# Kernel optimization log

Hardware: AMD Instinct MI355X
Metric: run time of the kernel (lower is better)

The kernel has to match this reference:

```python
import jax, jax.numpy as jnp
import numpy as np

INPUT, HIDDEN, LINEAR, BATCH, SEQ = 300, 1024, 1024, 256, 128
EPS = 1e-5

def setup_inputs() -> dict:
    key = jax.random.key(0)
    ks = jax.random.split(key, 12)
    s_ih = 1.0 / np.sqrt(HIDDEN)
    inp = {
        "x": jax.random.normal(ks[0], (SEQ, BATCH, INPUT), dtype=jnp.float32),
        "W_ih": jax.random.uniform(ks[1], (4 * HIDDEN, INPUT), jnp.float32, -s_ih, s_ih),
        "W_hh": jax.random.uniform(ks[2], (4 * HIDDEN, HIDDEN), jnp.float32, -s_ih, s_ih),
        "b_ih": jax.random.uniform(ks[3], (4 * HIDDEN,), jnp.float32, -s_ih, s_ih),
        "b_hh": jax.random.uniform(ks[4], (4 * HIDDEN,), jnp.float32, -s_ih, s_ih),
        "W1": jax.random.uniform(ks[5], (LINEAR, HIDDEN), jnp.float32, -s_ih, s_ih),
        "b1": jax.random.uniform(ks[6], (LINEAR,), jnp.float32, -s_ih, s_ih),
        "gamma": jnp.ones((LINEAR,), jnp.float32),
        "beta": jnp.zeros((LINEAR,), jnp.float32),
        "W2": jax.random.uniform(ks[7], (1, LINEAR), jnp.float32, -1.0 / np.sqrt(LINEAR), 1.0 / np.sqrt(LINEAR)),
        "b2": jax.random.uniform(ks[8], (1,), jnp.float32, -1.0 / np.sqrt(LINEAR), 1.0 / np.sqrt(LINEAR)),
    }
    return inp

def reference(x, W_ih, W_hh, b_ih, b_hh, W1, b1, gamma, beta, W2, b2):
    # Stepwise LSTMCell loop (dropout path; training=False -> dropout is identity)
    B, H = x.shape[1], W_hh.shape[1]
    bias = b_ih + b_hh  # [4H]

    def step(carry, xt):
        h, c = carry
        gates = xt @ W_ih.T + h @ W_hh.T + bias  # [B, 4H]
        i, f, g, o = jnp.split(gates, 4, axis=-1)
        c = jax.nn.sigmoid(f) * c + jax.nn.sigmoid(i) * jnp.tanh(g)
        h = jax.nn.sigmoid(o) * jnp.tanh(c)
        return (h, c), None

    h0 = jnp.zeros((B, H), x.dtype)
    (h, _), _ = jax.lax.scan(step, (h0, h0), x)

    # head: linear -> BatchNorm1d (train-mode batch stats) -> relu -> linear
    z = h @ W1.T + b1  # [B, LINEAR]
    mean = jnp.mean(z, axis=0)
    var = jnp.var(z, axis=0)  # biased, matching torch BN training path
    z = (z - mean) * jax.lax.rsqrt(var + EPS) * gamma + beta
    z = jax.nn.relu(z)
    out = z @ W2.T + b2  # [B, 1]
    out = 3.0 * jax.nn.sigmoid(out)
    return out.squeeze(-1)  # [B]
```

## Files before the change

kernel.cpp:

```cpp
#include <hip/hip_runtime.h>
#include <math.h>

#define SEQ 128
#define BATCH 256
#define INPUT 300
#define HIDDEN 1024
#define NG 4096
#define KH 1024
#define KXP 320
#define KT 1344
#define NKT64 21
#define HT64 16
#define NKTH 32
#define LINEARN 1024
#define AROW 72
#define TILE_SH (64 * AROW)
#define BUF_SH (3 * TILE_SH)

typedef __attribute__((ext_vector_type(8))) short short8;
typedef __attribute__((ext_vector_type(4))) float floatx4;

__device__ __forceinline__ float sigf(float x)     { return 1.f / (1.f + __expf(-x)); }
__device__ __forceinline__ float tanhfast(float x) { return 2.f / (1.f + __expf(-2.f * x)) - 1.f; }

__device__ __forceinline__ unsigned short bf16_rne(float f) {
  unsigned u = __float_as_uint(f);
  u += 0x7FFFu + ((u >> 16) & 1u);
  return (unsigned short)(u >> 16);
}
__device__ __forceinline__ float bf16f(unsigned short s) {
  return __uint_as_float(((unsigned)s) << 16);
}

__device__ __forceinline__ void mfma3(floatx4& acc, short8 ah, short8 al, short8 bh, short8 bl) {
  acc = __builtin_amdgcn_mfma_f32_16x16x32_bf16(ah, bh, acc, 0, 0, 0);
  acc = __builtin_amdgcn_mfma_f32_16x16x32_bf16(ah, bl, acc, 0, 0, 0);
  acc = __builtin_amdgcn_mfma_f32_16x16x32_bf16(al, bh, acc, 0, 0, 0);
}
__device__ __forceinline__ void mfma2(floatx4& acc, short8 ah, short8 al, short8 bh) {
  acc = __builtin_amdgcn_mfma_f32_16x16x32_bf16(ah, bh, acc, 0, 0, 0);
  acc = __builtin_amdgcn_mfma_f32_16x16x32_bf16(al, bh, acc, 0, 0, 0);
}

__global__ __launch_bounds__(256) void zero_ws(float4* p, int n4) {
  int i = blockIdx.x * 256 + threadIdx.x;
  if (i < n4) p[i] = make_float4(0.f, 0.f, 0.f, 0.f);
}

__global__ __launch_bounds__(256) void pack_w(
    const float* __restrict__ W_ih, const float* __restrict__ W_hh,
    unsigned short* __restrict__ Wph)
{
  int id = blockIdx.x * 256 + threadIdx.x;
  if (id >= NG * KT) return;
  int n = id / KT;
  int k = id - n * KT;
  int j = n >> 2, g = n & 3;
  int srow = g * HIDDEN + j;
  float w = 0.f;
  if (k < KH) w = W_hh[(size_t)srow * HIDDEN + k];
  else if (k - KH < INPUT) w = W_ih[(size_t)srow * INPUT + (k - KH)];
  Wph[id] = bf16_rne(w);
}

__global__ __launch_bounds__(256) void pack_bias(
    const float* __restrict__ b_ih, const float* __restrict__ b_hh,
    float* __restrict__ biasp)
{
  int n = blockIdx.x * 256 + threadIdx.x;
  if (n >= NG) return;
  int j = n >> 2, g = n & 3;
  int s = g * HIDDEN + j;
  biasp[n] = b_ih[s] + b_hh[s];
}

__global__ __launch_bounds__(256) void pack_x(
    const float* __restrict__ x, unsigned short* __restrict__ xph,
    unsigned short* __restrict__ xpl)
{
  int id = blockIdx.x * 256 + threadIdx.x;
  if (id >= SEQ * BATCH * KXP) return;
  int row = id / KXP;
  int k = id - row * KXP;
  float v = (k < INPUT) ? x[(size_t)row * INPUT + k] : 0.f;
  unsigned short hi = bf16_rne(v);
  xph[id] = hi;
  xpl[id] = bf16_rne(v - bf16f(hi));
}

__global__ __launch_bounds__(256) void pack_w1(
    const float* __restrict__ W1, unsigned short* __restrict__ W1ph,
    unsigned short* __restrict__ W1pl)
{
  int id = blockIdx.x * 256 + threadIdx.x;
  if (id >= LINEARN * HIDDEN) return;
  float w = W1[id];
  unsigned short hi = bf16_rne(w);
  W1ph[id] = hi;
  W1pl[id] = bf16_rne(w - bf16f(hi));
}

__global__ __launch_bounds__(512) void lstm_step5(
    const unsigned short* __restrict__ xp_hi,
    const unsigned short* __restrict__ xp_lo,
    const unsigned short* __restrict__ h_hi_r,
    const unsigned short* __restrict__ h_lo_r,
    const unsigned short* __restrict__ Wph,
    const float* __restrict__ biasp,
    float* __restrict__ cst,
    unsigned short* __restrict__ h_hi_w,
    unsigned short* __restrict__ h_lo_w)
{
  __shared__ short sb[2 * BUF_SH];
  __shared__ float epi[64 * 65];

  const int t    = threadIdx.x;
  const int lane = t & 63;
  const int wave = t >> 6;
  const int wm   = (wave >> 2) * 32;
  const int wn   = (wave & 3) * 16;
  const int col  = lane & 15;
  const int quad = lane >> 4;
  const int r    = t >> 3;
  const int k8   = (t & 7) * 8;
  const int id     = blockIdx.x;
  const int jtile  = (id & 7) * 8 + ((id >> 3) & 7);
  const int mt_    = id >> 6;
  const int m0   = mt_ * 64;
  const int n0   = jtile * 64;
  const int j0   = jtile * 16;

  const int mloc = t >> 2;
  const int jl4  = (t & 3) * 4;
  float4 cold;
  if (t < 256) cold = *(const float4*)(cst + (size_t)(m0 + mloc) * HIDDEN + (j0 + jl4));

#define LOAD_TILE(kt, AH, AL, BH) do {                                       \
    if ((kt) < HT64) {                                                       \
      const int ka = (kt) * 64 + k8;                                         \
      AH = *(const uint4*)(h_hi_r + (size_t)(m0 + r) * KH + ka);             \
      AL = *(const uint4*)(h_lo_r + (size_t)(m0 + r) * KH + ka);             \
    } else {                                                                 \
      const int kx = ((kt) - HT64) * 64 + k8;                                \
      AH = *(const uint4*)(xp_hi + (size_t)(m0 + r) * KXP + kx);             \
      AL = *(const uint4*)(xp_lo + (size_t)(m0 + r) * KXP + kx);             \
    }                                                                        \
    BH = *(const uint4*)(Wph + (size_t)(n0 + r) * KT + (kt) * 64 + k8);      \
  } while (0)

#define STORE_TILE(base, AH, AL, BH) do {                                    \
    *(uint4*)((base) +               r * AROW + k8) = AH;                    \
    *(uint4*)((base) + TILE_SH     + r * AROW + k8) = AL;                    \
    *(uint4*)((base) + 2 * TILE_SH + r * AROW + k8) = BH;                    \
  } while (0)

  floatx4 acc[2];
  acc[0] = (floatx4){0.f, 0.f, 0.f, 0.f};
  acc[1] = (floatx4){0.f, 0.f, 0.f, 0.f};

  uint4 cAh, cAl, cBh, nAh, nAl, nBh, tAh, tAl, tBh;
  LOAD_TILE(0, tAh, tAl, tBh);
  LOAD_TILE(1, cAh, cAl, cBh);
  STORE_TILE(sb, tAh, tAl, tBh);

  const int arow0 = (wm + col) * AROW + quad * 8;
  const int arow1 = (wm + 16 + col) * AROW + quad * 8;
  const int brow  = (wn + col) * AROW + quad * 8;

  for (int kt = 0; kt < NKT64; ++kt) {
    if (kt + 2 < NKT64) LOAD_TILE(kt + 2, nAh, nAl, nBh);
    __syncthreads();
    const short* bufp = sb + (kt & 1) * BUF_SH;

#pragma unroll
    for (int sub = 0; sub < 2; ++sub) {
      const int so = sub * 32;
      const short8 bh = *(const short8*)(bufp + 2 * TILE_SH + brow + so);
      const short8 a0 = *(const short8*)(bufp + arow0 + so);
      const short8 l0 = *(const short8*)(bufp + TILE_SH + arow0 + so);
      const short8 a1 = *(const short8*)(bufp + arow1 + so);
      const short8 l1 = *(const short8*)(bufp + TILE_SH + arow1 + so);
      mfma2(acc[0], a0, l0, bh);
      mfma2(acc[1], a1, l1, bh);
    }

    if (kt + 1 < NKT64) STORE_TILE(sb + ((kt + 1) & 1) * BUF_SH, cAh, cAl, cBh);
    cAh = nAh; cAl = nAl; cBh = nBh;
  }
#undef LOAD_TILE
#undef STORE_TILE

  const float bb = biasp[n0 + wn + col];
#pragma unroll
  for (int mt = 0; mt < 2; ++mt) {
    const int nl = wn + col;
#pragma unroll
    for (int reg = 0; reg < 4; ++reg) {
      const int ml = wm + mt * 16 + quad * 4 + reg;
      epi[nl * 65 + ml] = acc[mt][reg] + bb;
    }
  }
  __syncthreads();

  if (t < 256) {
    float cn[4], hn[4];
#pragma unroll
    for (int jj = 0; jj < 4; ++jj) {
      const int nl = (jl4 + jj) * 4;
      const float gi = epi[(nl + 0) * 65 + mloc];
      const float gf = epi[(nl + 1) * 65 + mloc];
      const float gg = epi[(nl + 2) * 65 + mloc];
      const float go = epi[(nl + 3) * 65 + mloc];
      const float cc = (jj == 0) ? cold.x : (jj == 1) ? cold.y : (jj == 2) ? cold.z : cold.w;
      const float cnew = sigf(gf) * cc + sigf(gi) * tanhfast(gg);
      cn[jj] = cnew;
      hn[jj] = sigf(go) * tanhfast(cnew);
    }
    *(float4*)(cst + (size_t)(m0 + mloc) * HIDDEN + (j0 + jl4)) =
        make_float4(cn[0], cn[1], cn[2], cn[3]);
    ushort4 uh, ul;
    uh.x = bf16_rne(hn[0]); uh.y = bf16_rne(hn[1]);
    uh.z = bf16_rne(hn[2]); uh.w = bf16_rne(hn[3]);
    ul.x = bf16_rne(hn[0] - bf16f(uh.x));
    ul.y = bf16_rne(hn[1] - bf16f(uh.y));
    ul.z = bf16_rne(hn[2] - bf16f(uh.z));
    ul.w = bf16_rne(hn[3] - bf16f(uh.w));
    *(ushort4*)(h_hi_w + (size_t)(m0 + mloc) * HIDDEN + (j0 + jl4)) = uh;
    *(ushort4*)(h_lo_w + (size_t)(m0 + mloc) * HIDDEN + (j0 + jl4)) = ul;
  }
}

__global__ __launch_bounds__(256) void head_gemm(
    const unsigned short* __restrict__ Ah_,
    const unsigned short* __restrict__ Al_,
    const unsigned short* __restrict__ Bh_,
    const unsigned short* __restrict__ Bl_,
    const float* __restrict__ bias,
    float* __restrict__ C)
{
  __shared__ short sb[2 * 4 * 2560];

  const int t    = threadIdx.x;
  const int lane = t & 63;
  const int wave = t >> 6;
  const int wm   = (wave >> 1) * 32;
  const int wn   = (wave & 1) * 32;
  const int col  = lane & 15;
  const int quad = lane >> 4;
  const int r    = t >> 2;
  const int k8   = (t & 3) * 8;
  const int m0   = blockIdx.y * 64;
  const int n0   = blockIdx.x * 64;

#define LOAD_TILE(kt, AH, AL, BH, BL) do {                                   \
    const int ka = (kt) * 32 + k8;                                           \
    AH = *(const uint4*)(Ah_ + (size_t)(m0 + r) * KH + ka);                  \
    AL = *(const uint4*)(Al_ + (size_t)(m0 + r) * KH + ka);                  \
    BH = *(const uint4*)(Bh_ + (size_t)(n0 + r) * KH + ka);                  \
    BL = *(const uint4*)(Bl_ + (size_t)(n0 + r) * KH + ka);                  \
  } while (0)

#define STORE_TILE(base, AH, AL, BH, BL) do {                                \
    *(uint4*)((base) +        r * 40 + k8) = AH;                             \
    *(uint4*)((base) + 2560 + r * 40 + k8) = AL;                             \
    *(uint4*)((base) + 5120 + r * 40 + k8) = BH;                             \
    *(uint4*)((base) + 7680 + r * 40 + k8) = BL;                             \
  } while (0)

  floatx4 acc[2][2];
#pragma unroll
  for (int i = 0; i < 2; ++i)
#pragma unroll
    for (int jj = 0; jj < 2; ++jj)
      acc[i][jj] = (floatx4){0.f, 0.f, 0.f, 0.f};

  uint4 cAh, cAl, cBh, cBl, nAh, nAl, nBh, nBl, tAh, tAl, tBh, tBl;
  LOAD_TILE(0, tAh, tAl, tBh, tBl);
  LOAD_TILE(1, cAh, cAl, cBh, cBl);
  STORE_TILE(sb, tAh, tAl, tBh, tBl);

  for (int kt = 0; kt < NKTH; ++kt) {
    if (kt + 2 < NKTH) LOAD_TILE(kt + 2, nAh, nAl, nBh, nBl);
    __syncthreads();
    short* bufp = sb + (kt & 1) * 10240;

    short8 ah[2], al[2], bh[2], bl[2];
#pragma unroll
    for (int mt = 0; mt < 2; ++mt) {
      const int row = (wm + mt * 16 + col) * 40 + quad * 8;
      ah[mt] = *(const short8*)(bufp + row);
      al[mt] = *(const short8*)(bufp + 2560 + row);
    }
#pragma unroll
    for (int nt = 0; nt < 2; ++nt) {
      const int row = (wn + nt * 16 + col) * 40 + quad * 8;
      bh[nt] = *(const short8*)(bufp + 5120 + row);
      bl[nt] = *(const short8*)(bufp + 7680 + row);
    }
#pragma unroll
    for (int mt = 0; mt < 2; ++mt)
#pragma unroll
      for (int nt = 0; nt < 2; ++nt)
        mfma3(acc[mt][nt], ah[mt], al[mt], bh[nt], bl[nt]);

    if (kt + 1 < NKTH) STORE_TILE(sb + ((kt + 1) & 1) * 10240, cAh, cAl, cBh, cBl);
    cAh = nAh; cAl = nAl; cBh = nBh; cBl = nBl;
  }
#undef LOAD_TILE
#undef STORE_TILE

#pragma unroll
  for (int mt = 0; mt < 2; ++mt)
#pragma unroll
    for (int nt = 0; nt < 2; ++nt) {
      const int nl = n0 + wn + nt * 16 + col;
      const float bb = bias[nl];
#pragma unroll
      for (int reg = 0; reg < 4; ++reg) {
        const int ml = m0 + wm + mt * 16 + quad * 4 + reg;
        C[(size_t)ml * LINEARN + nl] = acc[mt][nt][reg] + bb;
      }
    }
}

__global__ __launch_bounds__(64) void bn_stats(
    const float* __restrict__ z, float* __restrict__ mean, float* __restrict__ rstd)
{
  const int n = blockIdx.x;
  const int t = threadIdx.x;
  float s = 0.f, s2 = 0.f;
  for (int r = t; r < BATCH; r += 64) {
    const float v = z[(size_t)r * LINEARN + n];
    s += v; s2 += v * v;
  }
#pragma unroll
  for (int off = 32; off > 0; off >>= 1) {
    s  += __shfl_down(s,  off, 64);
    s2 += __shfl_down(s2, off, 64);
  }
  if (t == 0) {
    const float mm = s * (1.f / BATCH);
    mean[n] = mm;
    rstd[n] = rsqrtf(s2 * (1.f / BATCH) - mm * mm + 1e-5f);
  }
}

__global__ __launch_bounds__(256) void head_out(
    const float* __restrict__ z, const float* __restrict__ mean, const float* __restrict__ rstd,
    const float* __restrict__ gamma, const float* __restrict__ beta,
    const float* __restrict__ W2, const float* __restrict__ b2, float* __restrict__ out)
{
  const int b = blockIdx.x;
  const int t = threadIdx.x;
  float acc = 0.f;
  for (int n = t; n < LINEARN; n += 256) {
    float v = (z[(size_t)b * LINEARN + n] - mean[n]) * rstd[n] * gamma[n] + beta[n];
    v = fmaxf(v, 0.f);
    acc += v * W2[n];
  }
#pragma unroll
  for (int off = 32; off > 0; off >>= 1) acc += __shfl_down(acc, off, 64);
  __shared__ float ls[4];
  if ((t & 63) == 0) ls[t >> 6] = acc;
  __syncthreads();
  if (t == 0) {
    const float tot = ls[0] + ls[1] + ls[2] + ls[3] + b2[0];
    out[b] = 3.f / (1.f + __expf(-tot));
  }
}

extern "C" void kernel_launch(void* const* d_in, const int* in_sizes, int n_in,
                              void* d_out, int out_size, void* d_ws, size_t ws_size,
                              hipStream_t stream) {
  const float* x     = (const float*)d_in[0];
  const float* W_ih  = (const float*)d_in[1];
  const float* W_hh  = (const float*)d_in[2];
  const float* b_ih  = (const float*)d_in[3];
  const float* b_hh  = (const float*)d_in[4];
  const float* W1    = (const float*)d_in[5];
  const float* b1    = (const float*)d_in[6];
  const float* gamma = (const float*)d_in[7];
  const float* beta  = (const float*)d_in[8];
  const float* W2    = (const float*)d_in[9];
  const float* b2    = (const float*)d_in[10];
  float* out = (float*)d_out;

  char* w = (char*)d_ws;
  unsigned short* h_hi0 = (unsigned short*)(w + 0);
  unsigned short* h_lo0 = (unsigned short*)(w + 524288);
  float*          cst   = (float*)(w + 1048576);
  unsigned short* h_hi1 = (unsigned short*)(w + 2097152);
  unsigned short* h_lo1 = (unsigned short*)(w + 2621440);
  unsigned short* Wph   = (unsigned short*)(w + 3145728);
  float*          biasp = (float*)(w + 14155776);
  unsigned short* xph   = (unsigned short*)(w + 14172160);
  unsigned short* xpl   = (unsigned short*)(w + 35143680);
  unsigned short* W1ph  = (unsigned short*)(w + 56115200);
  unsigned short* W1pl  = (unsigned short*)(w + 58212352);
  float*          z     = (float*)(w + 60309504);
  float*          mean  = (float*)(w + 61358080);
  float*          rstd  = (float*)(w + 61362176);

  zero_ws<<<512, 256, 0, stream>>>((float4*)w, 131072);
  pack_w<<<(NG * KT + 255) / 256, 256, 0, stream>>>(W_ih, W_hh, Wph);
  pack_bias<<<NG / 256, 256, 0, stream>>>(b_ih, b_hh, biasp);
  pack_x<<<(SEQ * BATCH * KXP + 255) / 256, 256, 0, stream>>>(x, xph, xpl);
  pack_w1<<<(LINEARN * HIDDEN + 255) / 256, 256, 0, stream>>>(W1, W1ph, W1pl);

  for (int t = 0; t < SEQ; ++t) {
    const unsigned short* hr_hi = (t & 1) ? h_hi1 : h_hi0;
    const unsigned short* hr_lo = (t & 1) ? h_lo1 : h_lo0;
    unsigned short* hw_hi = (t & 1) ? h_hi0 : h_hi1;
    unsigned short* hw_lo = (t & 1) ? h_lo0 : h_lo1;
    lstm_step5<<<256, 512, 0, stream>>>(
        xph + (size_t)t * BATCH * KXP, xpl + (size_t)t * BATCH * KXP,
        hr_hi, hr_lo, Wph, biasp, cst, hw_hi, hw_lo);
  }

  head_gemm<<<dim3(LINEARN / 64, BATCH / 64), 256, 0, stream>>>(
      h_hi0, h_lo0, W1ph, W1pl, b1, z);
  bn_stats<<<LINEARN, 64, 0, stream>>>(z, mean, rstd);
  head_out<<<BATCH, 256, 0, stream>>>(z, mean, rstd, gamma, beta, W2, b2, out);
}
```

Before: 1.850 ms.

## Double LSTM step K-tile to 128 and swap wave tiling to share A fragments

The per-step LSTM GEMM now stages 128-wide K tiles instead of 64, halving the number of barrier-synchronised iterations. The padded x width grows from 320 to 384 columns to fit the larger tile, and the workspace offsets are updated to match. Each wave now covers 16 rows by 32 gate columns, so one hi/lo A fragment is reused across two B fragments, cutting LDS reads per MFMA. In exchange, shared memory per block roughly doubles, which may reduce occupancy, and the extra zero padding in K adds some wasted MFMA work.

```diff
diff --git a/kernel.cpp b/kernel.cpp
--- a/kernel.cpp
+++ b/kernel.cpp
@@ -7,13 +7,13 @@
 #define HIDDEN 1024
 #define NG 4096
 #define KH 1024
-#define KXP 320
-#define KT 1344
-#define NKT64 21
-#define HT64 16
+#define KXP 384
+#define KT 1408
+#define NKT128 11
+#define HT128 8
 #define NKTH 32
 #define LINEARN 1024
-#define AROW 72
+#define AROW 136
 #define TILE_SH (64 * AROW)
 #define BUF_SH (3 * TILE_SH)
 
@@ -100,7 +100,7 @@
   W1pl[id] = bf16_rne(w - bf16f(hi));
 }
 
-__global__ __launch_bounds__(512) void lstm_step5(
+__global__ __launch_bounds__(512) void lstm_step6(
     const unsigned short* __restrict__ xp_hi,
     const unsigned short* __restrict__ xp_lo,
     const unsigned short* __restrict__ h_hi_r,
@@ -117,8 +117,8 @@
   const int t    = threadIdx.x;
   const int lane = t & 63;
   const int wave = t >> 6;
-  const int wm   = (wave >> 2) * 32;
-  const int wn   = (wave & 3) * 16;
+  const int wm   = (wave & 3) * 16;
+  const int wn   = (wave >> 2) * 32;
   const int col  = lane & 15;
   const int quad = lane >> 4;
   const int r    = t >> 3;
@@ -135,69 +135,80 @@
   float4 cold;
   if (t < 256) cold = *(const float4*)(cst + (size_t)(m0 + mloc) * HIDDEN + (j0 + jl4));
 
-#define LOAD_TILE(kt, AH, AL, BH) do {                                       \
-    if ((kt) < HT64) {                                                       \
-      const int ka = (kt) * 64 + k8;                                         \
-      AH = *(const uint4*)(h_hi_r + (size_t)(m0 + r) * KH + ka);             \
-      AL = *(const uint4*)(h_lo_r + (size_t)(m0 + r) * KH + ka);             \
+#define LOAD_TILE(kt, AH0, AH1, AL0, AL1, BH0, BH1) do {                     \
+    if ((kt) < HT128) {                                                      \
+      const int ka = (kt) * 128 + k8;                                        \
+      AH0 = *(const uint4*)(h_hi_r + (size_t)(m0 + r) * KH + ka);            \
+      AH1 = *(const uint4*)(h_hi_r + (size_t)(m0 + r) * KH + ka + 64);       \
+      AL0 = *(const uint4*)(h_lo_r + (size_t)(m0 + r) * KH + ka);            \
+      AL1 = *(const uint4*)(h_lo_r + (size_t)(m0 + r) * KH + ka + 64);       \
     } else {                                                                 \
-      const int kx = ((kt) - HT64) * 64 + k8;                                \
-      AH = *(const uint4*)(xp_hi + (size_t)(m0 + r) * KXP + kx);             \
-      AL = *(const uint4*)(xp_lo + (size_t)(m0 + r) * KXP + kx);             \
+      const int kx = ((kt) - HT128) * 128 + k8;                              \
+      AH0 = *(const uint4*)(xp_hi + (size_t)(m0 + r) * KXP + kx);            \
+      AH1 = *(const uint4*)(xp_hi + (size_t)(m0 + r) * KXP + kx + 64);       \
+      AL0 = *(const uint4*)(xp_lo + (size_t)(m0 + r) * KXP + kx);            \
+      AL1 = *(const uint4*)(xp_lo + (size_t)(m0 + r) * KXP + kx + 64);       \
     }                                                                        \
-    BH = *(const uint4*)(Wph + (size_t)(n0 + r) * KT + (kt) * 64 + k8);      \
+    BH0 = *(const uint4*)(Wph + (size_t)(n0 + r) * KT + (kt) * 128 + k8);    \
+    BH1 = *(const uint4*)(Wph + (size_t)(n0 + r) * KT + (kt) * 128 + k8 + 64);\
   } while (0)
 
-#define STORE_TILE(base, AH, AL, BH) do {                                    \
-    *(uint4*)((base) +               r * AROW + k8) = AH;                    \
-    *(uint4*)((base) + TILE_SH     + r * AROW + k8) = AL;                    \
-    *(uint4*)((base) + 2 * TILE_SH + r * AROW + k8) = BH;                    \
+#define STORE_TILE(base, AH0, AH1, AL0, AL1, BH0, BH1) do {                  \
+    *(uint4*)((base) +               r * AROW + k8)      = AH0;              \
+    *(uint4*)((base) +               r * AROW + k8 + 64) = AH1;              \
+    *(uint4*)((base) + TILE_SH     + r * AROW + k8)      = AL0;              \
+    *(uint4*)((base) + TILE_SH     + r * AROW + k8 + 64) = AL1;              \
+    *(uint4*)((base) + 2 * TILE_SH + r * AROW + k8)      = BH0;              \
+    *(uint4*)((base) + 2 * TILE_SH + r * AROW + k8 + 64) = BH1;              \
   } while (0)
 
   floatx4 acc[2];
   acc[0] = (floatx4){0.f, 0.f, 0.f, 0.f};
   acc[1] = (floatx4){0.f, 0.f, 0.f, 0.f};
 
-  uint4 cAh, cAl, cBh, nAh, nAl, nBh, tAh, tAl, tBh;
-  LOAD_TILE(0, tAh, tAl, tBh);
-  LOAD_TILE(1, cAh, cAl, cBh);
-  STORE_TILE(sb, tAh, tAl, tBh);
-
-  const int arow0 = (wm + col) * AROW + quad * 8;
-  const int arow1 = (wm + 16 + col) * AROW + quad * 8;
-  const int brow  = (wn + col) * AROW + quad * 8;
-
-  for (int kt = 0; kt < NKT64; ++kt) {
-    if (kt + 2 < NKT64) LOAD_TILE(kt + 2, nAh, nAl, nBh);
+  uint4 cA0, cA1, cL0, cL1, cB0, cB1;
+  uint4 nA0, nA1, nL0, nL1, nB0, nB1;
+  uint4 tA0, tA1, tL0, tL1, tB0, tB1;
+  LOAD_TILE(0, tA0, tA1, tL0, tL1, tB0, tB1);
+  LOAD_TILE(1, cA0, cA1, cL0, cL1, cB0, cB1);
+  STORE_TILE(sb, tA0, tA1, tL0, tL1, tB0, tB1);
+
+  const int arow  = (wm + col) * AROW + quad * 8;
+  const int brow0 = (wn + col) * AROW + quad * 8;
+  const int brow1 = (wn + 16 + col) * AROW + quad * 8;
+
+  for (int kt = 0; kt < NKT128; ++kt) {
+    if (kt + 2 < NKT128) LOAD_TILE(kt + 2, nA0, nA1, nL0, nL1, nB0, nB1);
     __syncthreads();
     const short* bufp = sb + (kt & 1) * BUF_SH;
 
 #pragma unroll
-    for (int sub = 0; sub < 2; ++sub) {
+    for (int sub = 0; sub < 4; ++sub) {
       const int so = sub * 32;
-      const short8 bh = *(const short8*)(bufp + 2 * TILE_SH + brow + so);
-      const short8 a0 = *(const short8*)(bufp + arow0 + so);
-      const short8 l0 = *(const short8*)(bufp + TILE_SH + arow0 + so);
-      const short8 a1 = *(const short8*)(bufp + arow1 + so);
-      const short8 l1 = *(const short8*)(bufp + TILE_SH + arow1 + so);
-      mfma2(acc[0], a0, l0, bh);
-      mfma2(acc[1], a1, l1, bh);
-    }
-
-    if (kt + 1 < NKT64) STORE_TILE(sb + ((kt + 1) & 1) * BUF_SH, cAh, cAl, cBh);
-    cAh = nAh; cAl = nAl; cBh = nBh;
+      const short8 a  = *(const short8*)(bufp + arow + so);
+      const short8 l  = *(const short8*)(bufp + TILE_SH + arow + so);
+      const short8 b0 = *(const short8*)(bufp + 2 * TILE_SH + brow0 + so);
+      const short8 b1 = *(const short8*)(bufp + 2 * TILE_SH + brow1 + so);
+      mfma2(acc[0], a, l, b0);
+      mfma2(acc[1], a, l, b1);
+    }
+
+    if (kt + 1 < NKT128) STORE_TILE(sb + ((kt + 1) & 1) * BUF_SH, cA0, cA1, cL0, cL1, cB0, cB1);
+    cA0 = nA0; cA1 = nA1; cL0 = nL0; cL1 = nL1; cB0 = nB0; cB1 = nB1;
   }
 #undef LOAD_TILE
 #undef STORE_TILE
 
-  const float bb = biasp[n0 + wn + col];
-#pragma unroll
-  for (int mt = 0; mt < 2; ++mt) {
-    const int nl = wn + col;
+  const float bias0 = biasp[n0 + wn + col];
+  const float bias1 = biasp[n0 + wn + 16 + col];
+#pragma unroll
+  for (int nt = 0; nt < 2; ++nt) {
+    const int nl = wn + nt * 16 + col;
+    const float bb = nt ? bias1 : bias0;
 #pragma unroll
     for (int reg = 0; reg < 4; ++reg) {
-      const int ml = wm + mt * 16 + quad * 4 + reg;
-      epi[nl * 65 + ml] = acc[mt][reg] + bb;
+      const int ml = wm + quad * 4 + reg;
+      epi[nl * 65 + ml] = acc[nt][reg] + bb;
     }
   }
   __syncthreads();
@@ -392,14 +403,14 @@
   unsigned short* h_hi1 = (unsigned short*)(w + 2097152);
   unsigned short* h_lo1 = (unsigned short*)(w + 2621440);
   unsigned short* Wph   = (unsigned short*)(w + 3145728);
-  float*          biasp = (float*)(w + 14155776);
-  unsigned short* xph   = (unsigned short*)(w + 14172160);
-  unsigned short* xpl   = (unsigned short*)(w + 35143680);
-  unsigned short* W1ph  = (unsigned short*)(w + 56115200);
-  unsigned short* W1pl  = (unsigned short*)(w + 58212352);
-  float*          z     = (float*)(w + 60309504);
-  float*          mean  = (float*)(w + 61358080);
-  float*          rstd  = (float*)(w + 61362176);
+  float*          biasp = (float*)(w + 14680064);
+  unsigned short* xph   = (unsigned short*)(w + 14696448);
+  unsigned short* xpl   = (unsigned short*)(w + 39862272);
+  unsigned short* W1ph  = (unsigned short*)(w + 65028096);
+  unsigned short* W1pl  = (unsigned short*)(w + 67125248);
+  float*          z     = (float*)(w + 69222400);
+  float*          mean  = (float*)(w + 70270976);
+  float*          rstd  = (float*)(w + 70275072);
 
   zero_ws<<<512, 256, 0, stream>>>((float4*)w, 131072);
   pack_w<<<(NG * KT + 255) / 256, 256, 0, stream>>>(W_ih, W_hh, Wph);
@@ -412,7 +423,7 @@
     const unsigned short* hr_lo = (t & 1) ? h_lo1 : h_lo0;
     unsigned short* hw_hi = (t & 1) ? h_hi0 : h_hi1;
     unsigned short* hw_lo = (t & 1) ? h_lo0 : h_lo1;
-    lstm_step5<<<256, 512, 0, stream>>>(
+    lstm_step6<<<256, 512, 0, stream>>>(
         xph + (size_t)t * BATCH * KXP, xpl + (size_t)t * BATCH * KXP,
         hr_hi, hr_lo, Wph, biasp, cst, hw_hi, hw_lo);
   }
```

After: 1.797 ms. -2.8%, faster.
